# Kernel tuning notes

Measured on AMD Instinct MI355X. Metric: run time of the kernel, lower is better.

Reference implementation:

```python
import jax, jax.numpy as jnp
import numpy as np

_DN = ('NCHW', 'OIHW', 'NCHW')

def _conv(x, w, stride=1, pad=1, dil=1, groups=1):
    return jax.lax.conv_general_dilated(
        x, w, window_strides=(stride, stride),
        padding=[(pad, pad), (pad, pad)],
        rhs_dilation=(dil, dil),
        feature_group_count=groups,
        dimension_numbers=_DN)


def setup_inputs() -> dict:
    key = jax.random.key(0)
    k1, k2, k3 = jax.random.split(key, 3)
    B, T, C_in, H, W = 4, 16, 32, 64, 64
    hidden = 64
    x = jax.random.normal(k1, (B, T, C_in, H, W), dtype=jnp.float32)
    # input-to-hidden conv weight: 3 gates stacked along out channels
    fan_i = C_in * 3 * 3
    W_i = jax.random.normal(k2, (3 * hidden, C_in, 3, 3), dtype=jnp.float32) / np.sqrt(fan_i)
    fan_h = hidden * 3 * 3
    W_h = jax.random.normal(k3, (3 * hidden, hidden, 3, 3), dtype=jnp.float32) / np.sqrt(fan_h)
    return {"x": x, "W_i": W_i, "W_h": W_h}


def reference(x, W_i, W_h):
    # x: [B, T, C_in, H, W] (batch_first). Single-layer unidirectional ConvGRU.
    B, T, C_in, H, Wd = x.shape
    hidden = W_h.shape[1]

    def cell(h, x_t):
        gi = _conv(x_t, W_i)          # [B, 3*hidden, H, W]
        gh = _conv(h, W_h)            # [B, 3*hidden, H, W]
        i_r, i_z, i_n = jnp.split(gi, 3, axis=1)
        h_r, h_z, h_n = jnp.split(gh, 3, axis=1)
        r = jax.nn.sigmoid(i_r + h_r)
        z = jax.nn.sigmoid(i_z + h_z)
        n = jnp.tanh(i_n + r * h_n)
        h_new = (1.0 - z) * n + z * h
        return h_new, h_new

    h0 = jnp.zeros((B, hidden, H, Wd), dtype=x.dtype)
    xs = jnp.moveaxis(x, 1, 0)        # [T, B, C_in, H, W]
    _, hs = jax.lax.scan(cell, h0, xs)
    return jnp.moveaxis(hs, 0, 1)     # [B, T, hidden, H, W]
```

## Files before the change

kernel.cpp:

```cpp
#include <hip/hip_runtime.h>
#include <math.h>

typedef unsigned short us;
typedef __attribute__((ext_vector_type(8))) short bf16x8;
typedef __attribute__((ext_vector_type(4))) float f32x4;

constexpr int B_  = 4;
constexpr int T_  = 16;
constexpr int CIN = 32;
constexpr int HID = 64;
constexpr int HH  = 64;
constexpr int WW  = 64;
constexpr int HW  = HH * WW;

constexpr int CSL = 40;
constexpr int KCH = 32;
constexpr int ASLAB_HW = 3 * 36 * 16 * 8;
constexpr int ATOTAL   = 12 * ASLAB_HW;
constexpr int ROW_HW   = 66 * CSL;
constexpr int PIMG_HW  = 66 * ROW_HW;
constexpr int T6_HW  = 6 * 18 * CSL;
constexpr int T6_GR  = T6_HW / 8;

constexpr size_t XT_OFF   = (size_t)ATOTAL;
constexpr size_t XT_HW    = (size_t)64 * PIMG_HW;
constexpr size_t HT_OFF   = XT_OFF + XT_HW;
constexpr size_t HTBUF_HW = (size_t)8 * PIMG_HW;
constexpr size_t WS_NEED_BYTES = (HT_OFF + 2 * HTBUF_HW) * 2;

constexpr int PB_XFILL = 66 * 64;
constexpr int PB_WCONV = (ATOTAL + 255) / 256;
constexpr int HZ_GRAN  = (int)(2 * HTBUF_HW / 8);
constexpr int PB_HZERO = (HZ_GRAN + 255) / 256;
constexpr int PB_TOTAL = PB_XFILL + PB_WCONV + PB_HZERO;

#define GLOAD_LDS16(gsrc, ldst) \
  __builtin_amdgcn_global_load_lds((const __attribute__((address_space(1))) void*)(gsrc), \
                                   (__attribute__((address_space(3))) void*)(ldst), 16, 0, 0)
#define MFMA_B(d, A, Bv) d = __builtin_amdgcn_mfma_f32_16x16x32_bf16(A, Bv, d, 0, 0, 0)

__device__ inline us f2bf(float f) {
    union { float f; unsigned u; } v; v.f = f;
    return (us)((v.u + 0x7FFFu + ((v.u >> 16) & 1u)) >> 16);
}
__device__ inline float bf2f(us h) {
    union { unsigned u; float f; } v; v.u = (unsigned)h << 16; return v.f;
}

__global__ void prep(const float* __restrict__ x,
                     const float* __restrict__ Wi, const float* __restrict__ Wh,
                     us* __restrict__ A2, us* __restrict__ xT, us* __restrict__ hT) {
    __shared__ float lds[64 * 41];
    const int bid = blockIdx.x;

    if (bid < PB_XFILL) {
        const int riT = bid % 66;
        const int bt  = bid / 66;
        us* dst = xT + (size_t)bt * PIMG_HW + (size_t)riT * ROW_HW;
        const bool interior = (riT >= 1 && riT <= 64);
        if (interior) {
            const float* src = x + (size_t)bt * 32 * HW + (riT - 1) * WW;
            const int p = threadIdx.x & 63;
            #pragma unroll
            for (int j = 0; j < 8; ++j) {
                int c = j * 4 + (threadIdx.x >> 6);
                lds[p * 41 + c] = src[c * HW + p];
            }
        }
        __syncthreads();
        for (int g = threadIdx.x; g < ROW_HW / 8; g += 256) {
            bf16x8 vv;
            #pragma unroll
            for (int k = 0; k < 8; ++k) {
                int off = g * 8 + k;
                int px = off / CSL, slot = off - px * CSL;
                float v = 0.f;
                if (interior && slot < 32 && px >= 1 && px <= 64)
                    v = lds[(px - 1) * 41 + slot];
                vv[k] = (short)f2bf(v);
            }
            *(bf16x8*)(dst + g * 8) = vv;
        }
    } else if (bid < PB_XFILL + PB_WCONV) {
        int idx = (bid - PB_XFILL) * 256 + threadIdx.x;
        if (idx >= ATOTAL) return;
        int ic  = idx & 31;
        int r1  = idx >> 5;
        int tap = r1 % 9;
        int r2  = r1 / 9;
        int m   = r2 & 15;
        int r3  = r2 >> 4;
        int gt  = r3 % 3;
        int r4  = r3 / 3;
        int hg  = r4 & 3;
        int ch  = r4 >> 2;
        int o   = gt * 64 + hg * 16 + m;
        float w = (ch == 0) ? Wi[(o * CIN + ic) * 9 + tap]
                            : Wh[(o * HID + (ch - 1) * 32 + ic) * 9 + tap];
        size_t dst = (size_t)(ch * 4 + hg) * ASLAB_HW
                   + ((size_t)(gt * 36 + tap * 4 + (ic >> 3)) * 16 + m) * 8 + (ic & 7);
        A2[dst] = f2bf(w);
    } else {
        int i = (bid - PB_XFILL - PB_WCONV) * 256 + threadIdx.x;
        if (i < HZ_GRAN) ((f32x4*)hT)[i] = f32x4{0.f, 0.f, 0.f, 0.f};
    }
}

__global__ __launch_bounds__(256, 1) void convgru_step(
    const us* __restrict__ xT, const us* __restrict__ A2,
    const us* __restrict__ hTrd, us* __restrict__ hTwr,
    float* __restrict__ out, int t)
{
    __shared__ __align__(16) us t0s[T6_HW];
    __shared__ __align__(16) us t1s[T6_HW];
    __shared__ __align__(16) us t2s[T6_HW];

    const int tid  = threadIdx.x;
    const int lane = tid & 63, hg = tid >> 6;
    const int px   = lane & 15, kl = lane >> 4;
    const int tile = blockIdx.x, ty = tile >> 2, tx = tile & 3, b = blockIdx.z;
    const int gy0 = ty * 4, gx0 = tx * 16;
    const int rowbase = gy0 * 66 + gx0;

    f32x4 aR[2][2], aZ[2][2], aNX[2][2], aNH[2][2];
    #pragma unroll
    for (int u = 0; u < 2; ++u)
        #pragma unroll
        for (int g = 0; g < 2; ++g) {
            aR[u][g] = f32x4{0.f,0.f,0.f,0.f}; aZ[u][g] = f32x4{0.f,0.f,0.f,0.f};
            aNX[u][g] = f32x4{0.f,0.f,0.f,0.f}; aNH[u][g] = f32x4{0.f,0.f,0.f,0.f};
        }
    bf16x8 a[27];

    auto stage_tin = [&](const us* src, us* dst) {
        #pragma unroll
        for (int j = 0; j < 3; ++j) {
            int G = tid + j * 256;
            if (G < T6_GR) {
                int r = G / 90, w = G - 90 * r;
                GLOAD_LDS16(src + (size_t)(rowbase + r * 66) * CSL + w * 8, dst + G * 8);
            }
        }
    };
    auto regA = [&](int ch) {
        const us* s = A2 + (size_t)(ch * 4 + hg) * ASLAB_HW + lane * 8;
        #pragma unroll
        for (int i = 0; i < 27; ++i)
            a[i] = *(const bf16x8*)(s + (size_t)((i / 9) * 36 + (i % 9) * 4) * 128);
    };

    const int rbase = px * CSL + kl * 8;

    auto compute = [&](const us* tb, bool isX, const us* nextA) {
        #pragma unroll
        for (int dx = 0; dx < 3; ++dx) {
            bf16x8 P[6];
            #pragma unroll
            for (int r = 0; r < 6; ++r)
                P[r] = *(const bf16x8*)(tb + (r * 18 + dx) * CSL + rbase);
            #pragma unroll
            for (int dy = 0; dy < 3; ++dy) {
                const int tap = dy * 3 + dx;
                bf16x8 ar = a[tap], az = a[9 + tap], an = a[18 + tap];
                if (nextA) {
                    a[tap]      = *(const bf16x8*)(nextA + (size_t)(0 * 36 + tap * 4) * 128);
                    a[9 + tap]  = *(const bf16x8*)(nextA + (size_t)(1 * 36 + tap * 4) * 128);
                    a[18 + tap] = *(const bf16x8*)(nextA + (size_t)(2 * 36 + tap * 4) * 128);
                }
                #pragma unroll
                for (int u = 0; u < 2; ++u) {
                    bf16x8 b0 = P[2 * u + dy], b1 = P[2 * u + dy + 1];
                    MFMA_B(aR[u][0], ar, b0); MFMA_B(aR[u][1], ar, b1);
                    MFMA_B(aZ[u][0], az, b0); MFMA_B(aZ[u][1], az, b1);
                    if (isX) { MFMA_B(aNX[u][0], an, b0); MFMA_B(aNX[u][1], an, b1); }
                    else     { MFMA_B(aNH[u][0], an, b0); MFMA_B(aNH[u][1], an, b1); }
                }
            }
        }
    };

    stage_tin(xT + (size_t)(b * T_ + t) * PIMG_HW, t0s);
    if (t > 0) {
        stage_tin(hTrd + (size_t)(b * 2 + 0) * PIMG_HW, t1s);
        stage_tin(hTrd + (size_t)(b * 2 + 1) * PIMG_HW, t2s);
    }
    regA(0);
    __syncthreads();

    const us* A1p = (t > 0) ? A2 + (size_t)(1 * 4 + hg) * ASLAB_HW + lane * 8 : nullptr;
    const us* A2p = (t > 0) ? A2 + (size_t)(2 * 4 + hg) * ASLAB_HW + lane * 8 : nullptr;

    compute(t0s, true, A1p);
    if (t > 0) {
        compute(t1s, false, A2p);
        compute(t2s, false, nullptr);
    }

    float* outp = out + ((size_t)(b * T_ + t)) * HID * HW;
    const int c0   = hg * 16 + kl * 4;
    const int slot = c0 & 31;
    const us* hbuf = (hg < 2) ? t1s : t2s;
    #pragma unroll
    for (int u = 0; u < 2; ++u) {
        #pragma unroll
        for (int g = 0; g < 2; ++g) {
            int orow = 2 * u + g;
            int gy = gy0 + orow, gx = gx0 + px;
            float hvf[4] = {0.f, 0.f, 0.f, 0.f};
            if (t > 0) {
                const us* hp = hbuf + (size_t)((orow + 1) * 18 + (px + 1)) * CSL + slot;
                #pragma unroll
                for (int q = 0; q < 4; ++q) hvf[q] = bf2f(hp[q]);
            }
            us hv[4];
            #pragma unroll
            for (int q = 0; q < 4; ++q) {
                float sr = __builtin_amdgcn_rcpf(1.f + __expf(-aR[u][g][q]));
                float sz = __builtin_amdgcn_rcpf(1.f + __expf(-aZ[u][g][q]));
                float ag = aNX[u][g][q] + sr * aNH[u][g][q];
                float nn = 2.f * __builtin_amdgcn_rcpf(1.f + __expf(-2.f * ag)) - 1.f;
                float hn = nn + sz * (hvf[q] - nn);
                outp[(size_t)(c0 + q) * HW + gy * WW + gx] = hn;
                hv[q] = f2bf(hn);
            }
            us* hd = hTwr + (size_t)(b * 2 + (c0 >> 5)) * PIMG_HW
                   + (size_t)((gy + 1) * 66 + (gx + 1)) * CSL + slot;
            *(uint2*)hd = *(const uint2*)hv;
        }
    }
}

constexpr int F_AROWB = 640;
constexpr int R4_ASLAB = 48 * 9 * KCH;
constexpr int R4_AVEC  = R4_ASLAB / 8;
constexpr int R4_ATOT  = 12 * R4_ASLAB;
constexpr int FPR = 10, FPC = 18;
__global__ void wconv_r4(const float* __restrict__ Wi, const float* __restrict__ Wh,
                         us* __restrict__ A2) {
    int idx = blockIdx.x * 256 + threadIdx.x;
    if (idx >= R4_ATOT) return;
    int ic = idx & 31; int r1 = idx >> 5;
    int tap = r1 % 9; int r2 = r1 / 9;
    int m = r2 & 15; int r3 = r2 >> 4;
    int gt = r3 % 3; int r4 = r3 / 3;
    int hg = r4 & 3; int ch = r4 >> 2;
    int o = gt * 64 + hg * 16 + m;
    float w = (ch == 0) ? Wi[(o * CIN + ic) * 9 + tap]
                        : Wh[(o * HID + (ch - 1) * 32 + ic) * 9 + tap];
    A2[idx] = f2bf(w);
}
__global__ __launch_bounds__(256, 2) void convgru_r4(
    const float* __restrict__ x, const us* __restrict__ A2,
    const float* hall, float* out, int t)
{
    __shared__ __align__(16) us tin[FPR * FPC * 40];
    __shared__ __align__(16) us Alr[48 * (F_AROWB / 2)];
    const int tid = threadIdx.x;
    const int lane = tid & 63, wave = tid >> 6;
    const int px = lane & 15, kl = lane >> 4;
    const int ty = blockIdx.x >> 2, tx = blockIdx.x & 3;
    const int hg = blockIdx.y, b = blockIdx.z;
    const int gy0 = ty * 8, gx0 = tx * 16;
    const int nch = (t > 0) ? 3 : 1;
    const float* hb = (t > 0) ? (hall + ((size_t)(b * T_ + t - 1)) * HID * HW) : nullptr;
    const float* xb = x + ((size_t)(b * T_ + t)) * CIN * HW;
    f32x4 accR[2] = {}, accZ[2] = {}, accNX[2] = {}, accNH[2] = {};
    float ireg[23]; bf16x8 areg[7];
    auto load_in = [&](int ch) {
        const float* src = (ch == 0) ? xb : (hb + (size_t)(ch - 1) * 32 * HW);
        #pragma unroll
        for (int j = 0; j < 23; ++j) {
            int e = tid + j * 256; float v = 0.f;
            if (e < FPR * FPC * 32) {
                int ic = e / (FPR * FPC); int rem = e - ic * (FPR * FPC);
                int r = rem / FPC, c = rem - r * FPC;
                int gy = gy0 + r - 1, gx = gx0 + c - 1;
                if ((unsigned)gy < (unsigned)HH && (unsigned)gx < (unsigned)WW)
                    v = src[ic * HW + gy * WW + gx];
            }
            ireg[j] = v;
        }
    };
    auto load_Ar = [&](int ch) {
        const us* s = A2 + (size_t)(ch * 4 + hg) * R4_ASLAB;
        #pragma unroll
        for (int j = 0; j < 7; ++j) { int v = tid + j * 256; if (v < R4_AVEC) areg[j] = *(const bf16x8*)(s + v * 8); }
    };
    auto write_in = [&]() {
        #pragma unroll
        for (int j = 0; j < 23; ++j) {
            int e = tid + j * 256;
            if (e < FPR * FPC * 32) {
                int ic = e / (FPR * FPC); int rem = e - ic * (FPR * FPC);
                int r = rem / FPC, c = rem - r * FPC;
                tin[(r * FPC + c) * 40 + ic] = f2bf(ireg[j]);
            }
        }
    };
    auto write_Ar = [&]() {
        #pragma unroll
        for (int j = 0; j < 7; ++j) {
            int v = tid + j * 256;
            if (v < R4_AVEC) {
                int row = v / 36; int kb = (v - row * 36) * 16;
                char* dst = (char*)Alr + row * F_AROWB + (kb ^ ((row & 7) << 4));
                *(bf16x8*)dst = areg[j];
            }
        }
    };
    const int rb0 = ((wave * 2 + 0) * FPC + px) * 40 + kl * 8;
    const int rb1 = rb0 + FPC * 40;
    const int swA = (px & 7) << 4;
    auto compute = [&](bool isX) {
        #pragma unroll
        for (int tap = 0; tap < 9; ++tap) {
            const int dy = tap / 3, dx = tap - 3 * dy;
            const int toff = (dy * FPC + dx) * 40;
            bf16x8 b0 = *(const bf16x8*)(tin + rb0 + toff);
            bf16x8 b1 = *(const bf16x8*)(tin + rb1 + toff);
            const char* ab = (const char*)Alr + px * F_AROWB + ((tap * 64 + kl * 16) ^ swA);
            bf16x8 ar = *(const bf16x8*)(ab);
            bf16x8 az = *(const bf16x8*)(ab + 16 * F_AROWB);
            bf16x8 an = *(const bf16x8*)(ab + 32 * F_AROWB);
            MFMA_B(accR[0], ar, b0); MFMA_B(accR[1], ar, b1);
            MFMA_B(accZ[0], az, b0); MFMA_B(accZ[1], az, b1);
            if (isX) { MFMA_B(accNX[0], an, b0); MFMA_B(accNX[1], an, b1); }
            else     { MFMA_B(accNH[0], an, b0); MFMA_B(accNH[1], an, b1); }
        }
    };
    load_in(0); load_Ar(0); write_in(); write_Ar();
    __syncthreads();
    for (int ch = 0; ch < nch; ++ch) {
        if (ch + 1 < nch) { load_in(ch + 1); load_Ar(ch + 1); }
        compute(ch == 0);
        __syncthreads();
        if (ch + 1 < nch) { write_in(); write_Ar(); __syncthreads(); }
    }
    float* outp = out + ((size_t)(b * T_ + t)) * HID * HW;
    #pragma unroll
    for (int g = 0; g < 2; ++g) {
        int gy = gy0 + wave * 2 + g; int gx = gx0 + px;
        #pragma unroll
        for (int q = 0; q < 4; ++q) {
            int c = hg * 16 + kl * 4 + q;
            float sr = 1.f / (1.f + expf(-accR[g][q]));
            float sz = 1.f / (1.f + expf(-accZ[g][q]));
            float nn = tanhf(accNX[g][q] + sr * accNH[g][q]);
            float hv = hb ? hb[(size_t)c * HW + gy * WW + gx] : 0.f;
            outp[(size_t)c * HW + gy * WW + gx] = (1.f - sz) * nn + sz * hv;
        }
    }
}

extern "C" void kernel_launch(void* const* d_in, const int* in_sizes, int n_in,
                              void* d_out, int out_size, void* d_ws, size_t ws_size,
                              hipStream_t stream) {
    const float* x  = (const float*)d_in[0];
    const float* Wi = (const float*)d_in[1];
    const float* Wh = (const float*)d_in[2];
    float* out = (float*)d_out;

    if (ws_size >= WS_NEED_BYTES) {
        us* A2  = (us*)d_ws;
        us* xT  = A2 + XT_OFF;
        us* hT0 = A2 + HT_OFF;
        us* hT1 = hT0 + HTBUF_HW;

        prep<<<PB_TOTAL, 256, 0, stream>>>(x, Wi, Wh, A2, xT, hT0);
        for (int t = 0; t < T_; ++t) {
            us* rd = (t & 1) ? hT1 : hT0;
            us* wr = (t & 1) ? hT0 : hT1;
            convgru_step<<<dim3(64, 1, 4), 256, 0, stream>>>(xT, A2, rd, wr, out, t);
        }
    } else {
        us* A2 = (us*)d_ws;
        wconv_r4<<<(R4_ATOT + 255) / 256, 256, 0, stream>>>(Wi, Wh, A2);
        for (int t = 0; t < T_; ++t)
            convgru_r4<<<dim3(32, 4, 4), 256, 0, stream>>>(x, A2, out, out, t);
    }
}
```

Before: 152.3 us.

## Remap step kernel so each block covers all batches for one hidden group

The step kernel used to give each wavefront in a block one hidden-channel group for a single batch. It now gives each wavefront one batch and makes the hidden group the grid's y dimension, so the block stages the input and hidden-state tiles for all four batches into one larger shared array. The weight slab each block loads into registers is now the same for all its wavefronts, while the activation tiles are staged four times per block, which raises LDS use and staging traffic per block. Output stores also become nontemporal to avoid polluting the cache.

After: 157.6 us. +3.5%, slower.

```diff
diff --git a/kernel.cpp b/kernel.cpp
--- a/kernel.cpp
+++ b/kernel.cpp
@@ -111,14 +111,13 @@
     const us* __restrict__ hTrd, us* __restrict__ hTwr,
     float* __restrict__ out, int t)
 {
-    __shared__ __align__(16) us t0s[T6_HW];
-    __shared__ __align__(16) us t1s[T6_HW];
-    __shared__ __align__(16) us t2s[T6_HW];
+    __shared__ __align__(16) us tin[12 * T6_HW];
 
     const int tid  = threadIdx.x;
-    const int lane = tid & 63, hg = tid >> 6;
+    const int lane = tid & 63, b = tid >> 6;
     const int px   = lane & 15, kl = lane >> 4;
-    const int tile = blockIdx.x, ty = tile >> 2, tx = tile & 3, b = blockIdx.z;
+    const int tile = blockIdx.x, ty = tile >> 2, tx = tile & 3;
+    const int hg = blockIdx.y;
     const int gy0 = ty * 4, gx0 = tx * 16;
     const int rowbase = gy0 * 66 + gx0;
 
@@ -179,10 +178,15 @@
         }
     };
 
-    stage_tin(xT + (size_t)(b * T_ + t) * PIMG_HW, t0s);
+    #pragma unroll
+    for (int bb = 0; bb < 4; ++bb)
+        stage_tin(xT + (size_t)(bb * T_ + t) * PIMG_HW, tin + (size_t)(bb * 3) * T6_HW);
     if (t > 0) {
-        stage_tin(hTrd + (size_t)(b * 2 + 0) * PIMG_HW, t1s);
-        stage_tin(hTrd + (size_t)(b * 2 + 1) * PIMG_HW, t2s);
+        #pragma unroll
+        for (int bb = 0; bb < 4; ++bb) {
+            stage_tin(hTrd + (size_t)(bb * 2 + 0) * PIMG_HW, tin + (size_t)(bb * 3 + 1) * T6_HW);
+            stage_tin(hTrd + (size_t)(bb * 2 + 1) * PIMG_HW, tin + (size_t)(bb * 3 + 2) * T6_HW);
+        }
     }
     regA(0);
     __syncthreads();
@@ -190,16 +194,17 @@
     const us* A1p = (t > 0) ? A2 + (size_t)(1 * 4 + hg) * ASLAB_HW + lane * 8 : nullptr;
     const us* A2p = (t > 0) ? A2 + (size_t)(2 * 4 + hg) * ASLAB_HW + lane * 8 : nullptr;
 
-    compute(t0s, true, A1p);
+    const us* myt = tin + (size_t)(b * 3) * T6_HW;
+    compute(myt, true, A1p);
     if (t > 0) {
-        compute(t1s, false, A2p);
-        compute(t2s, false, nullptr);
+        compute(myt + T6_HW, false, A2p);
+        compute(myt + 2 * T6_HW, false, nullptr);
     }
 
     float* outp = out + ((size_t)(b * T_ + t)) * HID * HW;
     const int c0   = hg * 16 + kl * 4;
     const int slot = c0 & 31;
-    const us* hbuf = (hg < 2) ? t1s : t2s;
+    const us* hbuf = (hg < 2) ? (myt + T6_HW) : (myt + 2 * T6_HW);
     #pragma unroll
     for (int u = 0; u < 2; ++u) {
         #pragma unroll
@@ -220,7 +225,7 @@
                 float ag = aNX[u][g][q] + sr * aNH[u][g][q];
                 float nn = 2.f * __builtin_amdgcn_rcpf(1.f + __expf(-2.f * ag)) - 1.f;
                 float hn = nn + sz * (hvf[q] - nn);
-                outp[(size_t)(c0 + q) * HW + gy * WW + gx] = hn;
+                __builtin_nontemporal_store(hn, &outp[(size_t)(c0 + q) * HW + gy * WW + gx]);
                 hv[q] = f2bf(hn);
             }
             us* hd = hTwr + (size_t)(b * 2 + (c0 >> 5)) * PIMG_HW
@@ -370,7 +375,7 @@
         for (int t = 0; t < T_; ++t) {
             us* rd = (t & 1) ? hT1 : hT0;
             us* wr = (t & 1) ? hT0 : hT1;
-            convgru_step<<<dim3(64, 1, 4), 256, 0, stream>>>(xT, A2, rd, wr, out, t);
+            convgru_step<<<dim3(64, 4, 1), 256, 0, stream>>>(xT, A2, rd, wr, out, t);
         }
     } else {
         us* A2 = (us*)d_ws;
```
